# Kernel optimization log

Measured on AMD Instinct MI355X. Metric: run time of the kernel, lower is better.

Reference implementation:

```python
import jax, jax.numpy as jnp
import numpy as np

N, IN, HID, OUT = 18432, 1024, 4096, 4096


def _quantize_per_channel(w):
    # symmetric per-output-channel int8 quantization: scale = max|w|/127
    scale = jnp.max(jnp.abs(w), axis=1) / 127.0  # [rows]
    scale = jnp.maximum(scale, 1e-8)
    w_int8 = jnp.clip(jnp.round(w / scale[:, None]), -127, 127).astype(jnp.int8)
    return w_int8, scale.astype(jnp.float32)


def setup_inputs() -> dict:
    key = jax.random.key(0)
    kx, k1, kb1, k2, kb2 = jax.random.split(key, 5)
    x = jax.random.normal(kx, (N, IN), dtype=jnp.float32)
    # kaiming-uniform-ish float weights, then per-channel int8 quantize
    bound1 = 1.0 / np.sqrt(IN)
    bound2 = 1.0 / np.sqrt(HID)
    w1 = jax.random.uniform(k1, (HID, IN), minval=-bound1, maxval=bound1, dtype=jnp.float32)
    w2 = jax.random.uniform(k2, (OUT, HID), minval=-bound2, maxval=bound2, dtype=jnp.float32)
    w1_int8, w1_scale = _quantize_per_channel(w1)
    w2_int8, w2_scale = _quantize_per_channel(w2)
    b1 = jax.random.uniform(kb1, (HID,), minval=-bound1, maxval=bound1, dtype=jnp.float32)
    b2 = jax.random.uniform(kb2, (OUT,), minval=-bound2, maxval=bound2, dtype=jnp.float32)
    return {"x": x, "w1_int8": w1_int8, "w1_scale": w1_scale, "b1": b1,
            "w2_int8": w2_int8, "w2_scale": w2_scale, "b2": b2}


def reference(x, w1_int8, w1_scale, b1, w2_int8, w2_scale, b2):
    # W8A16 dequant GEMM + fused GELU (layer 1)
    w1 = w1_int8.astype(jnp.float32) * w1_scale[:, None]  # [HID, IN]
    h = jax.nn.gelu(x @ w1.T + b1, approximate=False)      # [N, HID]
    # W8A16 dequant GEMM (layer 2)
    w2 = w2_int8.astype(jnp.float32) * w2_scale[:, None]  # [OUT, HID]
    return h @ w2.T + b2                                   # [N, OUT]
```

## Files before the change

### kernel.cpp

```cpp
#include <hip/hip_runtime.h>
#include <math.h>

#define NROWS 18432
#define IN_DIM 1024
#define HID_DIM 4096
#define OUT_DIM 4096
#define NTN 16
#define BM  192

typedef __attribute__((ext_vector_type(8))) short bf16x8;
typedef __attribute__((ext_vector_type(4))) float f32x4;

typedef const __attribute__((address_space(1))) char gchar;
typedef __attribute__((address_space(3))) char lchar;

__device__ __forceinline__ unsigned short f2bf(float f) {
    union { float f; unsigned u; } v; v.f = f;
    unsigned r = v.u + 0x7fffu + ((v.u >> 16) & 1u);
    return (unsigned short)(r >> 16);
}

__device__ __forceinline__ f32x4 MFMA16(bf16x8 a, bf16x8 b, f32x4 c) {
    return __builtin_amdgcn_mfma_f32_16x16x32_bf16(a, b, c, 0, 0, 0);
}


__global__ void cvt_f32_bf16_k(const float4* __restrict__ in, uint4* __restrict__ out, int nvec) {
    int i = blockIdx.x * blockDim.x + threadIdx.x;
    if (i >= nvec) return;
    float4 a = in[2 * i], b = in[2 * i + 1];
    union { unsigned short s[8]; uint4 v; } o;
    o.s[0] = f2bf(a.x); o.s[1] = f2bf(a.y); o.s[2] = f2bf(a.z); o.s[3] = f2bf(a.w);
    o.s[4] = f2bf(b.x); o.s[5] = f2bf(b.y); o.s[6] = f2bf(b.z); o.s[7] = f2bf(b.w);
    out[i] = o.v;
}

__global__ void cvt_i32_bf16_k(const int4* __restrict__ in, uint4* __restrict__ out, int nvec) {
    int i = blockIdx.x * blockDim.x + threadIdx.x;
    if (i >= nvec) return;
    int4 a = in[2 * i], b = in[2 * i + 1];
    union { unsigned short s[8]; uint4 v; } o;
    o.s[0] = f2bf((float)a.x); o.s[1] = f2bf((float)a.y);
    o.s[2] = f2bf((float)a.z); o.s[3] = f2bf((float)a.w);
    o.s[4] = f2bf((float)b.x); o.s[5] = f2bf((float)b.y);
    o.s[6] = f2bf((float)b.z); o.s[7] = f2bf((float)b.w);
    out[i] = o.v;
}

template<int EPI>
__global__ __launch_bounds__(512, 2)
void gemm192(const unsigned short* __restrict__ A, const unsigned short* __restrict__ B,
             const float* __restrict__ scale, const float* __restrict__ bias,
             void* __restrict__ Cout, int K) {
    extern __shared__ __align__(16) char sm[];

    const int tid  = threadIdx.x;
    const int lane = tid & 63;
    const int wid  = tid >> 6;
    const int wm   = wid >> 2, wn = wid & 3;

    const int nwg  = gridDim.x;
    const int q    = nwg >> 3, r = nwg & 7;
    const int xcd  = blockIdx.x & 7, bidx = blockIdx.x >> 3;
    const int swz  = xcd * q + (xcd < r ? xcd : r) + bidx;
    const int tm   = swz / NTN, tn = swz % NTN;

    const size_t rowbytes = (size_t)K * 2;
    const char* Ag = (const char*)A + (size_t)tm * BM * rowbytes;
    const char* Bg = (const char*)B + (size_t)tn * 256 * rowbytes;

    const int l16 = lane & 15;
    const int cgi = lane >> 4;
    const int sw  = l16 & 7;
    const int c0  = ((cgi       ^ sw) << 4);
    const int c1  = (((4 | cgi) ^ sw) << 4);

    f32x4  acc[6][4] = {};
    bf16x8 aq[3][2], bn0[2][2], bn1[2][2];

    const int NIT = K >> 7;

#define STAGE(GB, LDSOFF, UN, TILE) { \
    const int po_ = ((UN) << 13) + (tid << 4); \
    const int pr_ = po_ >> 7; \
    const int pc_ = (po_ & 127) ^ ((pr_ & 7) << 4); \
    __builtin_amdgcn_global_load_lds( \
        (gchar*)((GB) + (size_t)pr_ * rowbytes + ((size_t)(TILE) << 7) + (size_t)pc_), \
        (lchar*)(sm + (LDSOFF) + po_), 16, 0, 0); \
}

#define READ_A(BUFOFF, MH) { const char* Ab_ = sm + (BUFOFF); \
    _Pragma("unroll") for (int mm_ = 0; mm_ < 3; ++mm_) { \
        const int ro_ = (wm * 96 + (MH) * 48 + mm_ * 16 + l16) << 7; \
        aq[mm_][0] = *(const bf16x8*)(Ab_ + ro_ + c0); \
        aq[mm_][1] = *(const bf16x8*)(Ab_ + ro_ + c1); } }

#define READ_B(BUFOFF, NH, DST) { const char* Bb_ = sm + (BUFOFF) + 24576; \
    _Pragma("unroll") for (int nn_ = 0; nn_ < 2; ++nn_) { \
        const int ro_ = ((wn >> 1) * 128 + (wn & 1) * 64 + (NH) * 32 + nn_ * 16 + l16) << 7; \
        DST[nn_][0] = *(const bf16x8*)(Bb_ + ro_ + c0); \
        DST[nn_][1] = *(const bf16x8*)(Bb_ + ro_ + c1); } }

#define MF(MH, NH, BQ) { __builtin_amdgcn_s_setprio(1); \
    _Pragma("unroll") for (int mm_ = 0; mm_ < 3; ++mm_) \
        _Pragma("unroll") for (int nn_ = 0; nn_ < 2; ++nn_) { \
            acc[(MH)*3+mm_][(NH)*2+nn_] = MFMA16(aq[mm_][0], BQ[nn_][0], acc[(MH)*3+mm_][(NH)*2+nn_]); \
            acc[(MH)*3+mm_][(NH)*2+nn_] = MFMA16(aq[mm_][1], BQ[nn_][1], acc[(MH)*3+mm_][(NH)*2+nn_]); } \
    __builtin_amdgcn_s_setprio(0); }

#define SFENCE __builtin_amdgcn_sched_barrier(0)
#define WAITV4 { SFENCE; asm volatile("s_waitcnt vmcnt(4)"); SFENCE; }
#define WAITV0 { SFENCE; asm volatile("s_waitcnt vmcnt(0)"); SFENCE; }
#define BARR   { SFENCE; __builtin_amdgcn_s_barrier(); SFENCE; }

#define BUF1 57344

    STAGE(Ag, 0,            0, 0); STAGE(Ag, 0,            1, 0); STAGE(Ag, 0,            2, 0);
    STAGE(Bg, 24576,        0, 0); STAGE(Bg, 24576,        1, 0);
    STAGE(Bg, 24576,        2, 0); STAGE(Bg, 24576,        3, 0);
    STAGE(Bg, BUF1 + 24576, 0, 1); STAGE(Bg, BUF1 + 24576, 1, 1);
    STAGE(Bg, BUF1 + 24576, 2, 1); STAGE(Bg, BUF1 + 24576, 3, 1);
    WAITV4; BARR;

    const int NT = K >> 6;
    for (int j = 0; j < NIT; ++j) {
        const int  t0 = 2 * j, t1 = 2 * j + 1;
        const bool lastj = (j == NIT - 1);

        READ_A(0, 0); READ_B(0, 0, bn0);
        STAGE(Ag, BUF1, 0, t1); STAGE(Ag, BUF1, 1, t1);
        BARR; MF(0, 0, bn0);
        READ_B(0, 1, bn1);
        STAGE(Ag, BUF1, 2, t1);
        BARR; MF(0, 1, bn1);
        READ_A(0, 1);
        if (!lastj) { STAGE(Bg, 24576, 0, t0 + 2); STAGE(Bg, 24576, 1, t0 + 2); }
        BARR; MF(1, 1, bn1);
        if (!lastj) { STAGE(Bg, 24576, 2, t0 + 2); STAGE(Bg, 24576, 3, t0 + 2); WAITV4; }
        else        { WAITV0; }
        BARR; MF(1, 0, bn0);
        READ_A(BUF1, 0); READ_B(BUF1, 0, bn0);
        if (!lastj) { STAGE(Ag, 0, 0, t0 + 2); STAGE(Ag, 0, 1, t0 + 2); }
        BARR; MF(0, 0, bn0);
        READ_B(BUF1, 1, bn1);
        if (!lastj) STAGE(Ag, 0, 2, t0 + 2);
        BARR; MF(0, 1, bn1);
        READ_A(BUF1, 1);
        if (!lastj) { STAGE(Bg, BUF1 + 24576, 0, t1 + 2); STAGE(Bg, BUF1 + 24576, 1, t1 + 2); }
        BARR; MF(1, 1, bn1);
        if (!lastj) { STAGE(Bg, BUF1 + 24576, 2, t1 + 2); STAGE(Bg, BUF1 + 24576, 3, t1 + 2);
                      WAITV4; }
        BARR; MF(1, 0, bn0);
    }
#undef STAGE
#undef READ_A
#undef READ_B
#undef MF
#undef SFENCE
#undef WAITV4
#undef WAITV0
#undef BARR
#undef BUF1

    const int rg = (lane >> 4) << 2;
    #pragma unroll
    for (int nq = 0; nq < 4; ++nq) {
        const int col = tn * 256 + wn * 64 + (nq >> 1) * 32 + (nq & 1) * 16 + l16;
        const float sc = scale[col];
        const float bi = bias[col];
        #pragma unroll
        for (int mq = 0; mq < 6; ++mq) {
            const int row0 = tm * BM + wm * 96 + (mq / 3) * 48 + (mq % 3) * 16 + rg;
            #pragma unroll
            for (int rr = 0; rr < 4; ++rr) {
                float v = acc[mq][nq][rr] * sc + bi;
                if (EPI == 0) {
                    float g = 0.5f * v * (1.0f + erff(v * 0.70710678118654752f));
                    ((unsigned short*)Cout)[(size_t)(row0 + rr) * 4096 + col] = f2bf(g);
                } else {
                    ((float*)Cout)[(size_t)(row0 + rr) * 4096 + col] = v;
                }
            }
        }
    }
}

extern "C" void kernel_launch(void* const* d_in, const int* in_sizes, int n_in,
                              void* d_out, int out_size, void* d_ws, size_t ws_size,
                              hipStream_t stream) {
    const float* x   = (const float*)d_in[0];
    const int*   w1q = (const int*)d_in[1];
    const float* s1  = (const float*)d_in[2];
    const float* b1  = (const float*)d_in[3];
    const int*   w2q = (const int*)d_in[4];
    const float* s2  = (const float*)d_in[5];
    const float* b2  = (const float*)d_in[6];
    float*       out = (float*)d_out;

    hipFuncSetAttribute((const void*)gemm192<0>, hipFuncAttributeMaxDynamicSharedMemorySize, 114688);
    hipFuncSetAttribute((const void*)gemm192<1>, hipFuncAttributeMaxDynamicSharedMemorySize, 114688);

    char* ws = (char*)d_ws;
    const size_t XBF  = (size_t)NROWS   * IN_DIM  * 2;
    const size_t W1BF = (size_t)HID_DIM * IN_DIM  * 2;
    const size_t W2BF = (size_t)OUT_DIM * HID_DIM * 2;
    const size_t FIXED = XBF + W1BF + W2BF;

    unsigned short* xbf  = (unsigned short*)ws;
    unsigned short* w1bf = (unsigned short*)(ws + XBF);
    unsigned short* w2bf = (unsigned short*)(ws + XBF + W1BF);
    unsigned short* hbuf = (unsigned short*)(ws + FIXED);

    {
        int nvx = NROWS * IN_DIM / 8;
        cvt_f32_bf16_k<<<(nvx + 255) / 256, 256, 0, stream>>>((const float4*)x, (uint4*)xbf, nvx);
        int nv1 = HID_DIM * IN_DIM / 8;
        cvt_i32_bf16_k<<<(nv1 + 255) / 256, 256, 0, stream>>>((const int4*)w1q, (uint4*)w1bf, nv1);
        int nv2 = OUT_DIM * HID_DIM / 8;
        cvt_i32_bf16_k<<<(nv2 + 255) / 256, 256, 0, stream>>>((const int4*)w2q, (uint4*)w2bf, nv2);
    }

    size_t avail = (ws_size > FIXED) ? (ws_size - FIXED) : 0;
    long rp = (long)(avail / ((size_t)HID_DIM * 2));
    rp = (rp / BM) * BM;
    if (rp > NROWS) rp = NROWS;
    if (rp < BM)    rp = BM;

    for (int r0 = 0; r0 < NROWS; r0 += (int)rp) {
        int rows = (int)(((long)(NROWS - r0) < rp) ? (NROWS - r0) : rp);
        dim3 g(NTN * (rows / BM));
        gemm192<0><<<g, 512, 114688, stream>>>(xbf + (size_t)r0 * IN_DIM, w1bf, s1, b1,
                                               (void*)hbuf, IN_DIM);
        gemm192<1><<<g, 512, 114688, stream>>>(hbuf, w2bf, s2, b2,
                                               (void*)(out + (size_t)r0 * OUT_DIM), HID_DIM);
    }
    (void)in_sizes; (void)n_in; (void)out_size;
}
```

Measured before the change: 801.7 us.

## Switch GEMM to 32x32x16 MFMA with fragment-ordered LDS staging

Replaces the 16x16x32 bf16 MFMA tiles with 32x32x16 MFMA tiles, so each wave computes 3x2 32x32 blocks. Global-to-LDS staging now writes data already arranged in per-lane MFMA fragment order, which lets LDS reads be contiguous per lane and drops the XOR swizzle. The goal is fewer MFMA issues and fewer LDS instructions per K-step, plus fewer bank conflicts. In exchange, the global loads become more scattered (each lane reads 16 bytes from a different row), and the epilogue store pattern changes.

New measurement: 988.8 us. 23.3% more time.

```diff
diff --git a/kernel.cpp b/kernel.cpp
--- a/kernel.cpp
+++ b/kernel.cpp
@@ -8,8 +8,8 @@
 #define NTN 16
 #define BM  192
 
-typedef __attribute__((ext_vector_type(8))) short bf16x8;
-typedef __attribute__((ext_vector_type(4))) float f32x4;
+typedef __attribute__((ext_vector_type(8)))  short bf16x8;
+typedef __attribute__((ext_vector_type(16))) float f32x16;
 
 typedef const __attribute__((address_space(1))) char gchar;
 typedef __attribute__((address_space(3))) char lchar;
@@ -20,8 +20,8 @@
     return (unsigned short)(r >> 16);
 }
 
-__device__ __forceinline__ f32x4 MFMA16(bf16x8 a, bf16x8 b, f32x4 c) {
-    return __builtin_amdgcn_mfma_f32_16x16x32_bf16(a, b, c, 0, 0, 0);
+__device__ __forceinline__ f32x16 MFMA32(bf16x8 a, bf16x8 b, f32x16 c) {
+    return __builtin_amdgcn_mfma_f32_32x32x16_bf16(a, b, c, 0, 0, 0);
 }
 
 
@@ -49,9 +49,9 @@
 
 template<int EPI>
 __global__ __launch_bounds__(512, 2)
-void gemm192(const unsigned short* __restrict__ A, const unsigned short* __restrict__ B,
-             const float* __restrict__ scale, const float* __restrict__ bias,
-             void* __restrict__ Cout, int K) {
+void gemmfc(const unsigned short* __restrict__ A, const unsigned short* __restrict__ B,
+            const float* __restrict__ scale, const float* __restrict__ bias,
+            void* __restrict__ Cout, int K) {
     extern __shared__ __align__(16) char sm[];
 
     const int tid  = threadIdx.x;
@@ -69,43 +69,30 @@
     const char* Ag = (const char*)A + (size_t)tm * BM * rowbytes;
     const char* Bg = (const char*)B + (size_t)tn * 256 * rowbytes;
 
-    const int l16 = lane & 15;
-    const int cgi = lane >> 4;
-    const int sw  = l16 & 7;
-    const int c0  = ((cgi       ^ sw) << 4);
-    const int c1  = (((4 | cgi) ^ sw) << 4);
-
-    f32x4  acc[6][4] = {};
-    bf16x8 aq[3][2], bn0[2][2], bn1[2][2];
+    const int l32 = lane & 31;
+
+    f32x16 acc0[3] = {};
+    f32x16 acc1[3] = {};
+    bf16x8 aq[4], b0[4], b1[4];
 
     const int NIT = K >> 7;
-
-#define STAGE(GB, LDSOFF, UN, TILE) { \
-    const int po_ = ((UN) << 13) + (tid << 4); \
-    const int pr_ = po_ >> 7; \
-    const int pc_ = (po_ & 127) ^ ((pr_ & 7) << 4); \
+    const int lb16 = lane << 4;
+
+#define STAGE(GB, REGOFF, UN, TILE) { \
+    const int fi_ = ((UN) << 3) + wid; \
+    const int rb_ = fi_ >> 2, kf_ = fi_ & 3; \
     __builtin_amdgcn_global_load_lds( \
-        (gchar*)((GB) + (size_t)pr_ * rowbytes + ((size_t)(TILE) << 7) + (size_t)pc_), \
-        (lchar*)(sm + (LDSOFF) + po_), 16, 0, 0); \
-}
-
-#define READ_A(BUFOFF, MH) { const char* Ab_ = sm + (BUFOFF); \
-    _Pragma("unroll") for (int mm_ = 0; mm_ < 3; ++mm_) { \
-        const int ro_ = (wm * 96 + (MH) * 48 + mm_ * 16 + l16) << 7; \
-        aq[mm_][0] = *(const bf16x8*)(Ab_ + ro_ + c0); \
-        aq[mm_][1] = *(const bf16x8*)(Ab_ + ro_ + c1); } }
-
-#define READ_B(BUFOFF, NH, DST) { const char* Bb_ = sm + (BUFOFF) + 24576; \
-    _Pragma("unroll") for (int nn_ = 0; nn_ < 2; ++nn_) { \
-        const int ro_ = ((wn >> 1) * 128 + (wn & 1) * 64 + (NH) * 32 + nn_ * 16 + l16) << 7; \
-        DST[nn_][0] = *(const bf16x8*)(Bb_ + ro_ + c0); \
-        DST[nn_][1] = *(const bf16x8*)(Bb_ + ro_ + c1); } }
-
-#define MF(MH, NH, BQ) { __builtin_amdgcn_s_setprio(1); \
-    _Pragma("unroll") for (int mm_ = 0; mm_ < 3; ++mm_) \
-        _Pragma("unroll") for (int nn_ = 0; nn_ < 2; ++nn_) { \
-            acc[(MH)*3+mm_][(NH)*2+nn_] = MFMA16(aq[mm_][0], BQ[nn_][0], acc[(MH)*3+mm_][(NH)*2+nn_]); \
-            acc[(MH)*3+mm_][(NH)*2+nn_] = MFMA16(aq[mm_][1], BQ[nn_][1], acc[(MH)*3+mm_][(NH)*2+nn_]); } \
+        (gchar*)((GB) + (size_t)(rb_ * 32 + l32) * rowbytes + ((size_t)(TILE) << 7) \
+                 + (size_t)((kf_ << 5) + ((lane >> 5) << 4))), \
+        (lchar*)(sm + (REGOFF) + (fi_ << 10) + lb16), 16, 0, 0); \
+}
+
+#define RA(BUFOFF, I, KF) (*(const bf16x8*)(sm + (BUFOFF) + (((wm * 3 + (I)) * 4 + (KF)) << 10) + lb16))
+#define RB(BUFOFF, J, KF) (*(const bf16x8*)(sm + (BUFOFF) + 24576 + (((wn * 2 + (J)) * 4 + (KF)) << 10) + lb16))
+
+#define MF(I) { __builtin_amdgcn_s_setprio(1); \
+    _Pragma("unroll") for (int kf_ = 0; kf_ < 4; ++kf_) acc0[I] = MFMA32(aq[kf_], b0[kf_], acc0[I]); \
+    _Pragma("unroll") for (int kf_ = 0; kf_ < 4; ++kf_) acc1[I] = MFMA32(aq[kf_], b1[kf_], acc1[I]); \
     __builtin_amdgcn_s_setprio(0); }
 
 #define SFENCE __builtin_amdgcn_sched_barrier(0)
@@ -122,39 +109,44 @@
     STAGE(Bg, BUF1 + 24576, 2, 1); STAGE(Bg, BUF1 + 24576, 3, 1);
     WAITV4; BARR;
 
-    const int NT = K >> 6;
     for (int j = 0; j < NIT; ++j) {
-        const int  t0 = 2 * j, t1 = 2 * j + 1;
+        const int  t1 = 2 * j + 1, ta2 = 2 * j + 2, tb2 = 2 * j + 3;
         const bool lastj = (j == NIT - 1);
 
-        READ_A(0, 0); READ_B(0, 0, bn0);
-        STAGE(Ag, BUF1, 0, t1); STAGE(Ag, BUF1, 1, t1);
-        BARR; MF(0, 0, bn0);
-        READ_B(0, 1, bn1);
-        STAGE(Ag, BUF1, 2, t1);
-        BARR; MF(0, 1, bn1);
-        READ_A(0, 1);
-        if (!lastj) { STAGE(Bg, 24576, 0, t0 + 2); STAGE(Bg, 24576, 1, t0 + 2); }
-        BARR; MF(1, 1, bn1);
-        if (!lastj) { STAGE(Bg, 24576, 2, t0 + 2); STAGE(Bg, 24576, 3, t0 + 2); WAITV4; }
+        #pragma unroll
+        for (int kf = 0; kf < 4; ++kf) {
+            aq[kf] = RA(0, 0, kf); b0[kf] = RB(0, 0, kf); b1[kf] = RB(0, 1, kf);
+        }
+        STAGE(Ag, BUF1, 0, t1); STAGE(Ag, BUF1, 1, t1); STAGE(Ag, BUF1, 2, t1);
+        BARR; MF(0);
+        #pragma unroll
+        for (int kf = 0; kf < 4; ++kf) aq[kf] = RA(0, 1, kf);
+        if (!lastj) { STAGE(Bg, 24576, 0, ta2); STAGE(Bg, 24576, 1, ta2); }
+        BARR; MF(1);
+        #pragma unroll
+        for (int kf = 0; kf < 4; ++kf) aq[kf] = RA(0, 2, kf);
+        if (!lastj) { STAGE(Bg, 24576, 2, ta2); STAGE(Bg, 24576, 3, ta2); WAITV4; }
         else        { WAITV0; }
-        BARR; MF(1, 0, bn0);
-        READ_A(BUF1, 0); READ_B(BUF1, 0, bn0);
-        if (!lastj) { STAGE(Ag, 0, 0, t0 + 2); STAGE(Ag, 0, 1, t0 + 2); }
-        BARR; MF(0, 0, bn0);
-        READ_B(BUF1, 1, bn1);
-        if (!lastj) STAGE(Ag, 0, 2, t0 + 2);
-        BARR; MF(0, 1, bn1);
-        READ_A(BUF1, 1);
-        if (!lastj) { STAGE(Bg, BUF1 + 24576, 0, t1 + 2); STAGE(Bg, BUF1 + 24576, 1, t1 + 2); }
-        BARR; MF(1, 1, bn1);
-        if (!lastj) { STAGE(Bg, BUF1 + 24576, 2, t1 + 2); STAGE(Bg, BUF1 + 24576, 3, t1 + 2);
-                      WAITV4; }
-        BARR; MF(1, 0, bn0);
+        BARR; MF(2);
+
+        #pragma unroll
+        for (int kf = 0; kf < 4; ++kf) {
+            aq[kf] = RA(BUF1, 0, kf); b0[kf] = RB(BUF1, 0, kf); b1[kf] = RB(BUF1, 1, kf);
+        }
+        if (!lastj) { STAGE(Ag, 0, 0, ta2); STAGE(Ag, 0, 1, ta2); STAGE(Ag, 0, 2, ta2); }
+        BARR; MF(0);
+        #pragma unroll
+        for (int kf = 0; kf < 4; ++kf) aq[kf] = RA(BUF1, 1, kf);
+        if (!lastj) { STAGE(Bg, BUF1 + 24576, 0, tb2); STAGE(Bg, BUF1 + 24576, 1, tb2); }
+        BARR; MF(1);
+        #pragma unroll
+        for (int kf = 0; kf < 4; ++kf) aq[kf] = RA(BUF1, 2, kf);
+        if (!lastj) { STAGE(Bg, BUF1 + 24576, 2, tb2); STAGE(Bg, BUF1 + 24576, 3, tb2); WAITV4; }
+        BARR; MF(2);
     }
 #undef STAGE
-#undef READ_A
-#undef READ_B
+#undef RA
+#undef RB
 #undef MF
 #undef SFENCE
 #undef WAITV4
@@ -162,27 +154,30 @@
 #undef BARR
 #undef BUF1
 
-    const int rg = (lane >> 4) << 2;
+    const int rbase = (lane >> 5) << 2;
     #pragma unroll
-    for (int nq = 0; nq < 4; ++nq) {
-        const int col = tn * 256 + wn * 64 + (nq >> 1) * 32 + (nq & 1) * 16 + l16;
-        const float sc = scale[col];
-        const float bi = bias[col];
-        #pragma unroll
-        for (int mq = 0; mq < 6; ++mq) {
-            const int row0 = tm * BM + wm * 96 + (mq / 3) * 48 + (mq % 3) * 16 + rg;
+    for (int i = 0; i < 3; ++i)
+        #pragma unroll
+        for (int jj = 0; jj < 2; ++jj) {
+            const f32x16* a = (jj == 0) ? &acc0[i] : &acc1[i];
+            const int col = tn * 256 + wn * 64 + jj * 32 + l32;
+            const float sc = scale[col];
+            const float bi = bias[col];
+            const int r0 = tm * BM + wm * 96 + i * 32 + rbase;
             #pragma unroll
-            for (int rr = 0; rr < 4; ++rr) {
-                float v = acc[mq][nq][rr] * sc + bi;
-                if (EPI == 0) {
-                    float g = 0.5f * v * (1.0f + erff(v * 0.70710678118654752f));
-                    ((unsigned short*)Cout)[(size_t)(row0 + rr) * 4096 + col] = f2bf(g);
-                } else {
-                    ((float*)Cout)[(size_t)(row0 + rr) * 4096 + col] = v;
+            for (int rg = 0; rg < 4; ++rg)
+                #pragma unroll
+                for (int rr = 0; rr < 4; ++rr) {
+                    float v = (*a)[rg * 4 + rr] * sc + bi;
+                    const int row = r0 + rg * 8 + rr;
+                    if (EPI == 0) {
+                        float g = 0.5f * v * (1.0f + erff(v * 0.70710678118654752f));
+                        ((unsigned short*)Cout)[(size_t)row * 4096 + col] = f2bf(g);
+                    } else {
+                        ((float*)Cout)[(size_t)row * 4096 + col] = v;
+                    }
                 }
-            }
         }
-    }
 }
 
 extern "C" void kernel_launch(void* const* d_in, const int* in_sizes, int n_in,
@@ -197,8 +192,8 @@
     const float* b2  = (const float*)d_in[6];
     float*       out = (float*)d_out;
 
-    hipFuncSetAttribute((const void*)gemm192<0>, hipFuncAttributeMaxDynamicSharedMemorySize, 114688);
-    hipFuncSetAttribute((const void*)gemm192<1>, hipFuncAttributeMaxDynamicSharedMemorySize, 114688);
+    hipFuncSetAttribute((const void*)gemmfc<0>, hipFuncAttributeMaxDynamicSharedMemorySize, 114688);
+    hipFuncSetAttribute((const void*)gemmfc<1>, hipFuncAttributeMaxDynamicSharedMemorySize, 114688);
 
     char* ws = (char*)d_ws;
     const size_t XBF  = (size_t)NROWS   * IN_DIM  * 2;
@@ -229,10 +224,10 @@
     for (int r0 = 0; r0 < NROWS; r0 += (int)rp) {
         int rows = (int)(((long)(NROWS - r0) < rp) ? (NROWS - r0) : rp);
         dim3 g(NTN * (rows / BM));
-        gemm192<0><<<g, 512, 114688, stream>>>(xbf + (size_t)r0 * IN_DIM, w1bf, s1, b1,
-                                               (void*)hbuf, IN_DIM);
-        gemm192<1><<<g, 512, 114688, stream>>>(hbuf, w2bf, s2, b2,
-                                               (void*)(out + (size_t)r0 * OUT_DIM), HID_DIM);
+        gemmfc<0><<<g, 512, 114688, stream>>>(xbf + (size_t)r0 * IN_DIM, w1bf, s1, b1,
+                                              (void*)hbuf, IN_DIM);
+        gemmfc<1><<<g, 512, 114688, stream>>>(hbuf, w2bf, s2, b2,
+                                              (void*)(out + (size_t)r0 * OUT_DIM), HID_DIM);
     }
     (void)in_sizes; (void)n_in; (void)out_size;
 }
```
